# Kernel optimization log

Measured on AMD Instinct MI355X. Metric: run time of the kernel, lower is better.

The kernel has to match this reference:

```python
import jax, jax.numpy as jnp
import numpy as np

N = 100000   # nodes
E = 1600000  # edges (avg degree 16)
D = 128      # in_dim == out_dim (residual path)
NEG_SLOPE = 0.1


def setup_inputs() -> dict:
    key = jax.random.key(0)
    k1, k2, k3 = jax.random.split(key, 3)
    x = jax.random.normal(k1, (N, D), dtype=jnp.float32)
    edge_index = jax.random.randint(k2, (2, E), 0, N, dtype=jnp.int32)
    # GCNConv linear weight (stored as [in, out]; PyG uses x @ W^T with [out, in] — same math)
    W = jax.random.normal(k3, (D, D), dtype=jnp.float32) / np.sqrt(D).astype(np.float32)
    b = jnp.zeros((D,), dtype=jnp.float32)
    return {"x": x, "edge_index": edge_index, "W": W, "b": b}


def reference(x, edge_index, W, b):
    n = x.shape[0]
    # add self loops (GCNConv add_self_loops=True)
    loops = jnp.arange(n, dtype=edge_index.dtype)
    src = jnp.concatenate([edge_index[0], loops])
    dst = jnp.concatenate([edge_index[1], loops])
    # symmetric normalization: deg computed on destination index (PyG gcn_norm)
    deg = jax.ops.segment_sum(jnp.ones_like(dst, dtype=x.dtype), dst, num_segments=n)
    dinv = jnp.where(deg > 0, jax.lax.rsqrt(deg), 0.0)
    norm = dinv[src] * dinv[dst]                     # [E+N]
    # transform-then-propagate: small GEMM, then gather/scale/scatter
    h = x @ W                                        # [N, D]
    msgs = h[src] * norm[:, None]                    # [E+N, D] gather + scale
    agg = jax.ops.segment_sum(msgs, dst, num_segments=n) + b  # scatter-add
    act = jnp.where(agg >= 0, agg, NEG_SLOPE * agg)  # leaky_relu(0.1)
    return act + x                                   # residual (in_dim == out_dim)
```

## Files before the change

kernel.cpp:

```cpp
#include <hip/hip_runtime.h>
#include <hip/hip_bf16.h>

#define D 128
#define NEG_SLOPE 0.1f
#define BSHIFT 7
#define BSIZE 128
#define SRCBITS 17
#define SRCMASK 0x1FFFF
#define NBMAX 784
#define REGION 2432

typedef __attribute__((ext_vector_type(8))) short bf16x8;
typedef __attribute__((ext_vector_type(4))) float f32x4;
typedef __attribute__((ext_vector_type(2))) float f32x2;

__device__ inline unsigned short f2bf(float f) {
    unsigned u = __builtin_bit_cast(unsigned, f);
    u += 0x7fff + ((u >> 16) & 1);
    return (unsigned short)(u >> 16);
}

__global__ __launch_bounds__(512) void k_scatter2(const int* __restrict__ src, const int* __restrict__ dst,
                                                  int* __restrict__ cursor, int* __restrict__ ebuf,
                                                  int E, int NB,
                                                  const float* __restrict__ W,
                                                  unsigned short* __restrict__ Wt) {
    int b = blockIdx.x;
    int nbE = gridDim.x - 32;
    if (b >= nbE) {
        int tt = (b - nbE) * 512 + threadIdx.x;
        int k = tt >> 7, nn = tt & 127;
        Wt[nn * D + k] = f2bf(W[k * D + nn]);
        return;
    }
    __shared__ int cntL[NBMAX], baseL[NBMAX], curL[NBMAX];
    int t = threadIdx.x;
    for (int i = t; i < NB; i += 512) { cntL[i] = 0; curL[i] = 0; }
    __syncthreads();

    const int4* src4 = (const int4*)src;
    const int4* dst4 = (const int4*)dst;
    int sv[8], dv[8];
#pragma unroll
    for (int j = 0; j < 2; j++) {
        int i4 = b * 1024 + j * 512 + t;
        int e = i4 * 4;
        int4 s, d;
        if (e + 4 <= E) {
            s = src4[i4];
            d = dst4[i4];
        } else {
            s.x = (e < E) ? src[e] : 0;     d.x = (e < E) ? dst[e] : -1;
            s.y = (e + 1 < E) ? src[e + 1] : 0; d.y = (e + 1 < E) ? dst[e + 1] : -1;
            s.z = (e + 2 < E) ? src[e + 2] : 0; d.z = (e + 2 < E) ? dst[e + 2] : -1;
            s.w = (e + 3 < E) ? src[e + 3] : 0; d.w = (e + 3 < E) ? dst[e + 3] : -1;
        }
        sv[j * 4 + 0] = s.x; sv[j * 4 + 1] = s.y; sv[j * 4 + 2] = s.z; sv[j * 4 + 3] = s.w;
        dv[j * 4 + 0] = d.x; dv[j * 4 + 1] = d.y; dv[j * 4 + 2] = d.z; dv[j * 4 + 3] = d.w;
    }
#pragma unroll
    for (int k = 0; k < 8; k++)
        if (dv[k] >= 0) atomicAdd(&cntL[dv[k] >> BSHIFT], 1);
    __syncthreads();
    for (int i = t; i < NB; i += 512) {
        int c = cntL[i];
        if (c) baseL[i] = atomicAdd(&cursor[i], c);
    }
    __syncthreads();
#pragma unroll
    for (int k = 0; k < 8; k++) {
        int d = dv[k];
        if (d >= 0) {
            int bk = d >> BSHIFT;
            int slot = baseL[bk] + atomicAdd(&curL[bk], 1);
            if (slot < REGION)
                ebuf[bk * REGION + slot] = ((d & (BSIZE - 1)) << SRCBITS) | sv[k];
        }
    }
}

__global__ __launch_bounds__(256) void k_gemm(const float* __restrict__ x,
                                              const unsigned short* __restrict__ Wt,
                                              const int* __restrict__ bucketCnt,
                                              const int* __restrict__ ebuf,
                                              unsigned char* __restrict__ h, int n) {
    __shared__ unsigned short Wl[D * 136];
    __shared__ int cntL[BSIZE];
    int t = threadIdx.x;
    if (t < BSIZE) cntL[t] = 0;
    const uint4* Wg4 = (const uint4*)Wt;
#pragma unroll
    for (int j = 0; j < 8; j++) {
        int c = t + 256 * j;
        int row = c >> 4, kg = c & 15;
        *(uint4*)&Wl[row * 136 + kg * 8] = Wg4[row * 16 + kg];
    }
    __syncthreads();

    int estart = blockIdx.x * REGION;
    int ecnt = bucketCnt[blockIdx.x];
    if (ecnt > REGION) ecnt = REGION;
    for (int e = t; e < ecnt; e += 256) atomicAdd(&cntL[ebuf[estart + e] >> SRCBITS], 1);

    int lane = t & 63, wave = t >> 6;
    int quad = lane >> 4, mrow = lane & 15;
    int rbase = blockIdx.x * 128 + wave * 32;

    const float4* x4 = (const float4*)x;
    float4 a0[2][4], a1[2][4];
#pragma unroll
    for (int rt = 0; rt < 2; rt++) {
        int row = rbase + rt * 16 + mrow;
        long rowl = (row < n) ? row : (n - 1);
#pragma unroll
        for (int ks = 0; ks < 4; ks++) {
            long base = rowl * 32 + ks * 8 + quad * 2;
            a0[rt][ks] = x4[base];
            a1[rt][ks] = x4[base + 1];
        }
    }
    bf16x8 af[2][4];
#pragma unroll
    for (int rt = 0; rt < 2; rt++)
#pragma unroll
        for (int ks = 0; ks < 4; ks++) {
            bf16x8 f;
            f[0] = (short)f2bf(a0[rt][ks].x); f[1] = (short)f2bf(a0[rt][ks].y);
            f[2] = (short)f2bf(a0[rt][ks].z); f[3] = (short)f2bf(a0[rt][ks].w);
            f[4] = (short)f2bf(a1[rt][ks].x); f[5] = (short)f2bf(a1[rt][ks].y);
            f[6] = (short)f2bf(a1[rt][ks].z); f[7] = (short)f2bf(a1[rt][ks].w);
            af[rt][ks] = f;
        }

    f32x4 acc[2][8];
#pragma unroll
    for (int rt = 0; rt < 2; rt++)
#pragma unroll
        for (int ct = 0; ct < 8; ct++) acc[rt][ct] = (f32x4){0.f, 0.f, 0.f, 0.f};

#pragma unroll
    for (int ks = 0; ks < 4; ks++) {
#pragma unroll
        for (int ct = 0; ct < 8; ct++) {
            bf16x8 bf = *(bf16x8*)&Wl[(ct * 16 + mrow) * 136 + ks * 32 + quad * 8];
#pragma unroll
            for (int rt = 0; rt < 2; rt++)
                acc[rt][ct] = __builtin_amdgcn_mfma_f32_16x16x32_bf16(af[rt][ks], bf, acc[rt][ct], 0, 0, 0);
        }
    }

    __syncthreads();

#pragma unroll
    for (int rt = 0; rt < 2; rt++) {
#pragma unroll
        for (int reg = 0; reg < 4; reg++) {
            int row = rbase + rt * 16 + quad * 4 + reg;
            if (row < n) {
                int rloc = wave * 32 + rt * 16 + quad * 4 + reg;
                float dv = rsqrtf((float)cntL[rloc] + 1.0f);
                float a[8];
#pragma unroll
                for (int ct = 0; ct < 8; ct++) a[ct] = acc[rt][ct][reg] * dv;
                int w0 = __builtin_amdgcn_cvt_pk_fp8_f32(a[0], a[1], 0, false);
                w0 = __builtin_amdgcn_cvt_pk_fp8_f32(a[2], a[3], w0, true);
                int w1 = __builtin_amdgcn_cvt_pk_fp8_f32(a[4], a[5], 0, false);
                w1 = __builtin_amdgcn_cvt_pk_fp8_f32(a[6], a[7], w1, true);
                uint2 wv; wv.x = (unsigned)w0; wv.y = (unsigned)w1;
                *(uint2*)&h[(long)row * 128 + mrow * 8] = wv;
            }
        }
    }
}

#define ACCV(v)                                                       \
    {                                                                 \
        acc2[0] += __builtin_amdgcn_cvt_pk_f32_fp8((int)(v).x, false);\
        acc2[1] += __builtin_amdgcn_cvt_pk_f32_fp8((int)(v).x, true); \
        acc2[2] += __builtin_amdgcn_cvt_pk_f32_fp8((int)(v).y, false);\
        acc2[3] += __builtin_amdgcn_cvt_pk_f32_fp8((int)(v).y, true); \
        acc2[4] += __builtin_amdgcn_cvt_pk_f32_fp8((int)(v).z, false);\
        acc2[5] += __builtin_amdgcn_cvt_pk_f32_fp8((int)(v).z, true); \
        acc2[6] += __builtin_amdgcn_cvt_pk_f32_fp8((int)(v).w, false);\
        acc2[7] += __builtin_amdgcn_cvt_pk_f32_fp8((int)(v).w, true); \
    }

__global__ __launch_bounds__(512) void k_aggregate(const uint4* __restrict__ h4, const float* __restrict__ x,
                                                   const float* __restrict__ bias,
                                                   const int* __restrict__ bucketCnt, const int* __restrict__ ebuf,
                                                   float* __restrict__ out, int N) {
    __shared__ int srcL[REGION];
    __shared__ int degL[BSIZE];
    __shared__ int startL[BSIZE];
    __shared__ int curL[BSIZE];

    int b = blockIdx.x;
    int t = threadIdx.x;
    int nstart = b << BSHIFT;
    int estart = b * REGION;
    int ecnt = bucketCnt[b];
    if (ecnt > REGION) ecnt = REGION;

    if (t < BSIZE) degL[t] = 0;
    __syncthreads();

    int ev[5];
#pragma unroll
    for (int k = 0; k < 5; k++) {
        int e = t + k * 512;
        ev[k] = (e < ecnt) ? ebuf[estart + e] : -1;
    }
#pragma unroll
    for (int k = 0; k < 5; k++)
        if (ev[k] >= 0) atomicAdd(&degL[ev[k] >> SRCBITS], 1);
    __syncthreads();

    if (t < 64) {
        int d0 = degL[2 * t], d1 = degL[2 * t + 1];
        int sum = d0 + d1;
        int inc = sum;
        for (int sh = 1; sh < 64; sh <<= 1) {
            int y = __shfl_up(inc, sh, 64);
            if (t >= sh) inc += y;
        }
        int e0 = inc - sum;
        startL[2 * t] = e0;
        startL[2 * t + 1] = e0 + d0;
        curL[2 * t] = e0;
        curL[2 * t + 1] = e0 + d0;
    }
    __syncthreads();
#pragma unroll
    for (int k = 0; k < 5; k++)
        if (ev[k] >= 0) {
            int v = ev[k];
            int pos = atomicAdd(&curL[v >> SRCBITS], 1);
            srcL[pos] = v & SRCMASK;
        }
    __syncthreads();

    int wave = t >> 6, lane = t & 63;
    int slot = lane >> 3, chunk = lane & 7;
    for (int nloc = wave; nloc < BSIZE; nloc += 8) {
        int i = nstart + nloc;
        if (i >= N) break;
        int start = startL[nloc], m = degL[nloc];

        f32x2 acc2[8];
#pragma unroll
        for (int r = 0; r < 8; r++) acc2[r] = (f32x2){0.f, 0.f};
        if (slot == 0) {
            uint4 v = h4[(long)i * 8 + chunk];
            ACCV(v);
        }

        int j0 = 0;
        if (m >= 16) {
            int ja = start + slot;
            int e0 = srcL[ja], e1 = srcL[ja + 8];
            for (;;) {
                uint4 v0 = h4[(long)e0 * 8 + chunk];
                uint4 v1 = h4[(long)e1 * 8 + chunk];
                j0 += 16;
                bool more = (j0 + 16 <= m);
                if (more) {
                    int jb = start + j0 + slot;
                    e0 = srcL[jb];
                    e1 = srcL[jb + 8];
                }
                ACCV(v0);
                ACCV(v1);
                if (!more) break;
            }
        }
        if (j0 + 8 <= m) {
            int e = srcL[start + j0 + slot];
            uint4 v = h4[(long)e * 8 + chunk];
            ACCV(v);
            j0 += 8;
        }
        for (int j = j0 + slot; j < m; j += 8) {
            int e = srcL[start + j];
            uint4 v = h4[(long)e * 8 + chunk];
            ACCV(v);
        }

#pragma unroll
        for (int r = 0; r < 8; r++) {
            acc2[r].x += __shfl_xor(acc2[r].x, 8, 64);
            acc2[r].x += __shfl_xor(acc2[r].x, 16, 64);
            acc2[r].x += __shfl_xor(acc2[r].x, 32, 64);
            acc2[r].y += __shfl_xor(acc2[r].y, 8, 64);
            acc2[r].y += __shfl_xor(acc2[r].y, 16, 64);
            acc2[r].y += __shfl_xor(acc2[r].y, 32, 64);
        }

        int s1 = slot >> 1;
        f32x2 eL = (s1 == 0) ? acc2[0] : (s1 == 1) ? acc2[1] : (s1 == 2) ? acc2[2] : acc2[3];
        f32x2 eH = (s1 == 0) ? acc2[4] : (s1 == 1) ? acc2[5] : (s1 == 2) ? acc2[6] : acc2[7];
        float ax = (slot & 1) ? eL.y : eL.x;
        float ay = (slot & 1) ? eH.y : eH.x;

        float di = rsqrtf((float)m + 1.0f);
        int dbase = slot * 16 + chunk * 2;
        float2 bb = *(const float2*)&bias[dbase];
        float2 xv = *(const float2*)&x[(long)i * D + dbase];
        ax = ax * di + bb.x;
        ay = ay * di + bb.y;
        ax = (ax >= 0.f) ? ax : NEG_SLOPE * ax;
        ay = (ay >= 0.f) ? ay : NEG_SLOPE * ay;
        float2 o;
        o.x = ax + xv.x;
        o.y = ay + xv.y;
        *(float2*)&out[(long)i * D + dbase] = o;
    }
}

extern "C" void kernel_launch(void* const* d_in, const int* in_sizes, int n_in,
                              void* d_out, int out_size, void* d_ws, size_t ws_size,
                              hipStream_t stream) {
    const float* x = (const float*)d_in[0];
    const int* edge_index = (const int*)d_in[1];
    const float* W = (const float*)d_in[2];
    const float* bias = (const float*)d_in[3];
    float* out = (float*)d_out;

    int N = in_sizes[0] / D;
    int E = in_sizes[1] / 2;
    const int* src = edge_index;
    const int* dst = edge_index + E;
    int NB = (N + BSIZE - 1) >> BSHIFT;

    char* ws = (char*)d_ws;
    size_t off = 0;
    auto alloc = [&](size_t bytes) {
        void* p = ws + off;
        off += (bytes + 15) & ~(size_t)15;
        return p;
    };
    int* cursor = (int*)alloc((size_t)NB * 4);
    int* ebuf = (int*)alloc((size_t)NB * REGION * 4);
    unsigned short* Wt = (unsigned short*)alloc((size_t)D * D * 2);
    unsigned char* h = (unsigned char*)alloc((size_t)N * D);

    int nbE = (E + 4095) / 4096;

    hipMemsetAsync(cursor, 0, (size_t)NB * 4, stream);
    k_scatter2<<<nbE + 32, 512, 0, stream>>>(src, dst, cursor, ebuf, E, NB, W, Wt);
    k_gemm<<<NB, 256, 0, stream>>>(x, Wt, cursor, ebuf, h, N);
    k_aggregate<<<NB, 512, 0, stream>>>((const uint4*)h, x, bias, cursor, ebuf, out, N);
}
```

Baseline: 217.7 us.

## Replace global atomic bucket cursors with per-block sorted runs and CSR build in GEMM

The edge scatter kernel now sorts each 8192-edge chunk locally in shared memory by destination bucket and writes contiguous runs plus per-bucket offsets, so the global cursor atomics and the memset go away. The GEMM kernel gathers its bucket's runs from every chunk, computes degrees, builds a per-node CSR (start, degree, sorted sources) and writes it out. The aggregate kernel becomes one wave per node that reads the prebuilt CSR. The intent is to remove global atomics and scattered writes and to spread aggregation across many small blocks. The cost is that each GEMM block scans about 196 run descriptors twice with serial per-thread loops, plus extra global CSR traffic.

```diff
diff --git a/kernel.cpp b/kernel.cpp
--- a/kernel.cpp
+++ b/kernel.cpp
@@ -8,7 +8,9 @@
 #define SRCBITS 17
 #define SRCMASK 0x1FFFF
 #define NBMAX 784
-#define REGION 2432
+#define NBPAD 1024
+#define EPB 8192
+#define REGION2 2432
 
 typedef __attribute__((ext_vector_type(8))) short bf16x8;
 typedef __attribute__((ext_vector_type(4))) float f32x4;
@@ -21,7 +23,7 @@
 }
 
 __global__ __launch_bounds__(512) void k_scatter2(const int* __restrict__ src, const int* __restrict__ dst,
-                                                  int* __restrict__ cursor, int* __restrict__ ebuf,
+                                                  int* __restrict__ runs, int* __restrict__ ebuf,
                                                   int E, int NB,
                                                   const float* __restrict__ W,
                                                   unsigned short* __restrict__ Wt) {
@@ -33,24 +35,29 @@
         Wt[nn * D + k] = f2bf(W[k * D + nn]);
         return;
     }
-    __shared__ int cntL[NBMAX], baseL[NBMAX], curL[NBMAX];
+    __shared__ int cntL[NBPAD];
+    __shared__ int baseL[NBPAD];
+    __shared__ int curL[NBMAX];
+    __shared__ int stageV[EPB];
+    __shared__ int wsum[8];
+
     int t = threadIdx.x;
-    for (int i = t; i < NB; i += 512) { cntL[i] = 0; curL[i] = 0; }
+    for (int i = t; i < NBPAD; i += 512) cntL[i] = 0;
     __syncthreads();
 
     const int4* src4 = (const int4*)src;
     const int4* dst4 = (const int4*)dst;
-    int sv[8], dv[8];
-#pragma unroll
-    for (int j = 0; j < 2; j++) {
-        int i4 = b * 1024 + j * 512 + t;
+    int sv[16], dv[16];
+#pragma unroll
+    for (int j = 0; j < 4; j++) {
+        int i4 = b * 2048 + j * 512 + t;
         int e = i4 * 4;
         int4 s, d;
         if (e + 4 <= E) {
             s = src4[i4];
             d = dst4[i4];
         } else {
-            s.x = (e < E) ? src[e] : 0;     d.x = (e < E) ? dst[e] : -1;
+            s.x = (e < E) ? src[e] : 0;         d.x = (e < E) ? dst[e] : -1;
             s.y = (e + 1 < E) ? src[e + 1] : 0; d.y = (e + 1 < E) ? dst[e + 1] : -1;
             s.z = (e + 2 < E) ? src[e + 2] : 0; d.z = (e + 2 < E) ? dst[e + 2] : -1;
             s.w = (e + 3 < E) ? src[e + 3] : 0; d.w = (e + 3 < E) ? dst[e + 3] : -1;
@@ -59,34 +66,71 @@
         dv[j * 4 + 0] = d.x; dv[j * 4 + 1] = d.y; dv[j * 4 + 2] = d.z; dv[j * 4 + 3] = d.w;
     }
 #pragma unroll
-    for (int k = 0; k < 8; k++)
+    for (int k = 0; k < 16; k++)
         if (dv[k] >= 0) atomicAdd(&cntL[dv[k] >> BSHIFT], 1);
     __syncthreads();
-    for (int i = t; i < NB; i += 512) {
-        int c = cntL[i];
-        if (c) baseL[i] = atomicAdd(&cursor[i], c);
-    }
-    __syncthreads();
-#pragma unroll
-    for (int k = 0; k < 8; k++) {
+
+    {
+        int lane = t & 63, wave = t >> 6;
+        int c0 = cntL[2 * t], c1 = cntL[2 * t + 1];
+        int sum = c0 + c1;
+        int inc = sum;
+        for (int sh = 1; sh < 64; sh <<= 1) {
+            int y = __shfl_up(inc, sh, 64);
+            if (lane >= sh) inc += y;
+        }
+        int texcl = inc - sum;
+        if (lane == 63) wsum[wave] = inc;
+        __syncthreads();
+        int woff = 0;
+        for (int w = 0; w < wave; w++) woff += wsum[w];
+        int e0 = woff + texcl;
+        baseL[2 * t] = e0;
+        baseL[2 * t + 1] = e0 + c0;
+        if (2 * t < NB) curL[2 * t] = e0;
+        if (2 * t + 1 < NB) curL[2 * t + 1] = e0 + c0;
+    }
+    __syncthreads();
+
+    long rrow = (long)b * (NB + 1);
+    for (int bb = t; bb < NB; bb += 512) runs[rrow + bb] = baseL[bb];
+    if (t == 0) {
+        int cnt = E - b * EPB;
+        if (cnt > EPB) cnt = EPB;
+        runs[rrow + NB] = cnt;
+    }
+
+#pragma unroll
+    for (int k = 0; k < 16; k++) {
         int d = dv[k];
         if (d >= 0) {
-            int bk = d >> BSHIFT;
-            int slot = baseL[bk] + atomicAdd(&curL[bk], 1);
-            if (slot < REGION)
-                ebuf[bk * REGION + slot] = ((d & (BSIZE - 1)) << SRCBITS) | sv[k];
-        }
-    }
+            int pos = atomicAdd(&curL[d >> BSHIFT], 1);
+            stageV[pos] = ((d & (BSIZE - 1)) << SRCBITS) | sv[k];
+        }
+    }
+    __syncthreads();
+
+    int4* eb4 = (int4*)&ebuf[(long)b * EPB];
+    const int4* st4 = (const int4*)stageV;
+#pragma unroll
+    for (int j = 0; j < 4; j++) eb4[j * 512 + t] = st4[j * 512 + t];
 }
 
 __global__ __launch_bounds__(256) void k_gemm(const float* __restrict__ x,
                                               const unsigned short* __restrict__ Wt,
-                                              const int* __restrict__ bucketCnt,
-                                              const int* __restrict__ ebuf,
-                                              unsigned char* __restrict__ h, int n) {
+                                              const int* __restrict__ runs, const int* __restrict__ ebuf,
+                                              int nbE,
+                                              int* __restrict__ startA, int* __restrict__ degA,
+                                              int* __restrict__ sorted_src,
+                                              unsigned char* __restrict__ h, int n, int NB) {
     __shared__ unsigned short Wl[D * 136];
     __shared__ int cntL[BSIZE];
+    __shared__ int startL[BSIZE];
+    __shared__ int curL[BSIZE];
+    __shared__ int srcL[REGION2];
+
     int t = threadIdx.x;
+    int b = blockIdx.x;
     if (t < BSIZE) cntL[t] = 0;
     const uint4* Wg4 = (const uint4*)Wt;
 #pragma unroll
@@ -97,14 +141,9 @@
     }
     __syncthreads();
 
-    int estart = blockIdx.x * REGION;
-    int ecnt = bucketCnt[blockIdx.x];
-    if (ecnt > REGION) ecnt = REGION;
-    for (int e = t; e < ecnt; e += 256) atomicAdd(&cntL[ebuf[estart + e] >> SRCBITS], 1);
-
     int lane = t & 63, wave = t >> 6;
     int quad = lane >> 4, mrow = lane & 15;
-    int rbase = blockIdx.x * 128 + wave * 32;
+    int rbase = b * 128 + wave * 32;
 
     const float4* x4 = (const float4*)x;
     float4 a0[2][4], a1[2][4];
@@ -119,6 +158,16 @@
             a1[rt][ks] = x4[base + 1];
         }
     }
+
+    int NBP = NB + 1;
+    for (int i = t; i < nbE; i += 256) {
+        long rrow = (long)i * NBP;
+        int rs = runs[rrow + b], re = runs[rrow + b + 1];
+        const int* ep = ebuf + (long)i * EPB;
+        for (int e = rs; e < re; e++) atomicAdd(&cntL[ep[e] >> SRCBITS], 1);
+    }
+    __syncthreads();
+
     bf16x8 af[2][4];
 #pragma unroll
     for (int rt = 0; rt < 2; rt++)
@@ -132,6 +181,46 @@
             af[rt][ks] = f;
         }
 
+    if (t < 64) {
+        int d0 = cntL[2 * t], d1 = cntL[2 * t + 1];
+        int sum = d0 + d1;
+        int inc = sum;
+        for (int sh = 1; sh < 64; sh <<= 1) {
+            int y = __shfl_up(inc, sh, 64);
+            if (t >= sh) inc += y;
+        }
+        int e0 = inc - sum;
+        startL[2 * t] = e0;
+        startL[2 * t + 1] = e0 + d0;
+        curL[2 * t] = e0;
+        curL[2 * t + 1] = e0 + d0;
+    }
+    __syncthreads();
+
+    if (t < BSIZE) {
+        int i = b * BSIZE + t;
+        if (i < n) {
+            startA[i] = b * REGION2 + startL[t];
+            degA[i] = cntL[t];
+        }
+    }
+
+    for (int i = t; i < nbE; i += 256) {
+        long rrow = (long)i * NBP;
+        int rs = runs[rrow + b], re = runs[rrow + b + 1];
+        const int* ep = ebuf + (long)i * EPB;
+        for (int e = rs; e < re; e++) {
+            int v = ep[e];
+            int pos = atomicAdd(&curL[v >> SRCBITS], 1);
+            if (pos < REGION2) srcL[pos] = v & SRCMASK;
+        }
+    }
+    __syncthreads();
+
+    int ecnt = startL[BSIZE - 1] + cntL[BSIZE - 1];
+    if (ecnt > REGION2) ecnt = REGION2;
+    for (int e = t; e < ecnt; e += 256) sorted_src[(long)b * REGION2 + e] = srcL[e];
+
     f32x4 acc[2][8];
 #pragma unroll
     for (int rt = 0; rt < 2; rt++)
@@ -148,8 +237,6 @@
                 acc[rt][ct] = __builtin_amdgcn_mfma_f32_16x16x32_bf16(af[rt][ks], bf, acc[rt][ct], 0, 0, 0);
         }
     }
-
-    __syncthreads();
 
 #pragma unroll
     for (int rt = 0; rt < 2; rt++) {
@@ -185,135 +272,84 @@
         acc2[7] += __builtin_amdgcn_cvt_pk_f32_fp8((int)(v).w, true); \
     }
 
-__global__ __launch_bounds__(512) void k_aggregate(const uint4* __restrict__ h4, const float* __restrict__ x,
+__global__ __launch_bounds__(256) void k_aggregate(const uint4* __restrict__ h4, const float* __restrict__ x,
                                                    const float* __restrict__ bias,
-                                                   const int* __restrict__ bucketCnt, const int* __restrict__ ebuf,
-                                                   float* __restrict__ out, int N) {
-    __shared__ int srcL[REGION];
-    __shared__ int degL[BSIZE];
-    __shared__ int startL[BSIZE];
-    __shared__ int curL[BSIZE];
-
-    int b = blockIdx.x;
-    int t = threadIdx.x;
-    int nstart = b << BSHIFT;
-    int estart = b * REGION;
-    int ecnt = bucketCnt[b];
-    if (ecnt > REGION) ecnt = REGION;
-
-    if (t < BSIZE) degL[t] = 0;
-    __syncthreads();
-
-    int ev[5];
-#pragma unroll
-    for (int k = 0; k < 5; k++) {
-        int e = t + k * 512;
-        ev[k] = (e < ecnt) ? ebuf[estart + e] : -1;
-    }
-#pragma unroll
-    for (int k = 0; k < 5; k++)
-        if (ev[k] >= 0) atomicAdd(&degL[ev[k] >> SRCBITS], 1);
-    __syncthreads();
-
-    if (t < 64) {
-        int d0 = degL[2 * t], d1 = degL[2 * t + 1];
-        int sum = d0 + d1;
-        int inc = sum;
-        for (int sh = 1; sh < 64; sh <<= 1) {
-            int y = __shfl_up(inc, sh, 64);
-            if (t >= sh) inc += y;
-        }
-        int e0 = inc - sum;
-        startL[2 * t] = e0;
-        startL[2 * t + 1] = e0 + d0;
-        curL[2 * t] = e0;
-        curL[2 * t + 1] = e0 + d0;
-    }
-    __syncthreads();
-#pragma unroll
-    for (int k = 0; k < 5; k++)
-        if (ev[k] >= 0) {
-            int v = ev[k];
-            int pos = atomicAdd(&curL[v >> SRCBITS], 1);
-            srcL[pos] = v & SRCMASK;
-        }
-    __syncthreads();
-
-    int wave = t >> 6, lane = t & 63;
+                                                   const int* __restrict__ startA, const int* __restrict__ degA,
+                                                   const int* __restrict__ sorted_src,
+                                                   float* __restrict__ out, int n) {
+    int wave = threadIdx.x >> 6, lane = threadIdx.x & 63;
+    int i = blockIdx.x * 4 + wave;
+    if (i >= n) return;
     int slot = lane >> 3, chunk = lane & 7;
-    for (int nloc = wave; nloc < BSIZE; nloc += 8) {
-        int i = nstart + nloc;
-        if (i >= N) break;
-        int start = startL[nloc], m = degL[nloc];
-
-        f32x2 acc2[8];
-#pragma unroll
-        for (int r = 0; r < 8; r++) acc2[r] = (f32x2){0.f, 0.f};
-        if (slot == 0) {
-            uint4 v = h4[(long)i * 8 + chunk];
-            ACCV(v);
-        }
-
-        int j0 = 0;
-        if (m >= 16) {
-            int ja = start + slot;
-            int e0 = srcL[ja], e1 = srcL[ja + 8];
-            for (;;) {
-                uint4 v0 = h4[(long)e0 * 8 + chunk];
-                uint4 v1 = h4[(long)e1 * 8 + chunk];
-                j0 += 16;
-                bool more = (j0 + 16 <= m);
-                if (more) {
-                    int jb = start + j0 + slot;
-                    e0 = srcL[jb];
-                    e1 = srcL[jb + 8];
-                }
-                ACCV(v0);
-                ACCV(v1);
-                if (!more) break;
+    int start = startA[i], m = degA[i];
+
+    f32x2 acc2[8];
+#pragma unroll
+    for (int r = 0; r < 8; r++) acc2[r] = (f32x2){0.f, 0.f};
+    if (slot == 0) {
+        uint4 v = h4[(long)i * 8 + chunk];
+        ACCV(v);
+    }
+
+    int j0 = 0;
+    if (m >= 16) {
+        int ja = start + slot;
+        int e0 = sorted_src[ja], e1 = sorted_src[ja + 8];
+        for (;;) {
+            uint4 v0 = h4[(long)e0 * 8 + chunk];
+            uint4 v1 = h4[(long)e1 * 8 + chunk];
+            j0 += 16;
+            bool more = (j0 + 16 <= m);
+            if (more) {
+                int jb = start + j0 + slot;
+                e0 = sorted_src[jb];
+                e1 = sorted_src[jb + 8];
             }
-        }
-        if (j0 + 8 <= m) {
-            int e = srcL[start + j0 + slot];
-            uint4 v = h4[(long)e * 8 + chunk];
-            ACCV(v);
-            j0 += 8;
-        }
-        for (int j = j0 + slot; j < m; j += 8) {
-            int e = srcL[start + j];
-            uint4 v = h4[(long)e * 8 + chunk];
-            ACCV(v);
-        }
-
-#pragma unroll
-        for (int r = 0; r < 8; r++) {
-            acc2[r].x += __shfl_xor(acc2[r].x, 8, 64);
-            acc2[r].x += __shfl_xor(acc2[r].x, 16, 64);
-            acc2[r].x += __shfl_xor(acc2[r].x, 32, 64);
-            acc2[r].y += __shfl_xor(acc2[r].y, 8, 64);
-            acc2[r].y += __shfl_xor(acc2[r].y, 16, 64);
-            acc2[r].y += __shfl_xor(acc2[r].y, 32, 64);
-        }
-
-        int s1 = slot >> 1;
-        f32x2 eL = (s1 == 0) ? acc2[0] : (s1 == 1) ? acc2[1] : (s1 == 2) ? acc2[2] : acc2[3];
-        f32x2 eH = (s1 == 0) ? acc2[4] : (s1 == 1) ? acc2[5] : (s1 == 2) ? acc2[6] : acc2[7];
-        float ax = (slot & 1) ? eL.y : eL.x;
-        float ay = (slot & 1) ? eH.y : eH.x;
-
-        float di = rsqrtf((float)m + 1.0f);
-        int dbase = slot * 16 + chunk * 2;
-        float2 bb = *(const float2*)&bias[dbase];
-        float2 xv = *(const float2*)&x[(long)i * D + dbase];
-        ax = ax * di + bb.x;
-        ay = ay * di + bb.y;
-        ax = (ax >= 0.f) ? ax : NEG_SLOPE * ax;
-        ay = (ay >= 0.f) ? ay : NEG_SLOPE * ay;
-        float2 o;
-        o.x = ax + xv.x;
-        o.y = ay + xv.y;
-        *(float2*)&out[(long)i * D + dbase] = o;
-    }
+            ACCV(v0);
+            ACCV(v1);
+            if (!more) break;
+        }
+    }
+    if (j0 + 8 <= m) {
+        int e = sorted_src[start + j0 + slot];
+        uint4 v = h4[(long)e * 8 + chunk];
+        ACCV(v);
+        j0 += 8;
+    }
+    for (int j = j0 + slot; j < m; j += 8) {
+        int e = sorted_src[start + j];
+        uint4 v = h4[(long)e * 8 + chunk];
+        ACCV(v);
+    }
+
+#pragma unroll
+    for (int r = 0; r < 8; r++) {
+        acc2[r].x += __shfl_xor(acc2[r].x, 8, 64);
+        acc2[r].x += __shfl_xor(acc2[r].x, 16, 64);
+        acc2[r].x += __shfl_xor(acc2[r].x, 32, 64);
+        acc2[r].y += __shfl_xor(acc2[r].y, 8, 64);
+        acc2[r].y += __shfl_xor(acc2[r].y, 16, 64);
+        acc2[r].y += __shfl_xor(acc2[r].y, 32, 64);
+    }
+
+    int s1 = slot >> 1;
+    f32x2 eL = (s1 == 0) ? acc2[0] : (s1 == 1) ? acc2[1] : (s1 == 2) ? acc2[2] : acc2[3];
+    f32x2 eH = (s1 == 0) ? acc2[4] : (s1 == 1) ? acc2[5] : (s1 == 2) ? acc2[6] : acc2[7];
+    float ax = (slot & 1) ? eL.y : eL.x;
+    float ay = (slot & 1) ? eH.y : eH.x;
+
+    float di = rsqrtf((float)m + 1.0f);
+    int dbase = slot * 16 + chunk * 2;
+    float2 bb = *(const float2*)&bias[dbase];
+    float2 xv = *(const float2*)&x[(long)i * D + dbase];
+    ax = ax * di + bb.x;
+    ay = ay * di + bb.y;
+    ax = (ax >= 0.f) ? ax : NEG_SLOPE * ax;
+    ay = (ay >= 0.f) ? ay : NEG_SLOPE * ay;
+    float2 o;
+    o.x = ax + xv.x;
+    o.y = ay + xv.y;
+    *(float2*)&out[(long)i * D + dbase] = o;
 }
 
 extern "C" void kernel_launch(void* const* d_in, const int* in_sizes, int n_in,
@@ -330,6 +366,7 @@
     const int* src = edge_index;
     const int* dst = edge_index + E;
     int NB = (N + BSIZE - 1) >> BSHIFT;
+    int nbE = (E + EPB - 1) / EPB;
 
     char* ws = (char*)d_ws;
     size_t off = 0;
@@ -338,15 +375,15 @@
         off += (bytes + 15) & ~(size_t)15;
         return p;
     };
-    int* cursor = (int*)alloc((size_t)NB * 4);
-    int* ebuf = (int*)alloc((size_t)NB * REGION * 4);
+    int* runs = (int*)alloc((size_t)nbE * (NB + 1) * 4);
+    int* ebuf = (int*)alloc((size_t)nbE * EPB * 4);
+    int* startA = (int*)alloc((size_t)N * 4);
+    int* degA = (int*)alloc((size_t)N * 4);
+    int* sorted_src = (int*)alloc((size_t)NB * REGION2 * 4);
     unsigned short* Wt = (unsigned short*)alloc((size_t)D * D * 2);
     unsigned char* h = (unsigned char*)alloc((size_t)N * D);
 
-    int nbE = (E + 4095) / 4096;
-
-    hipMemsetAsync(cursor, 0, (size_t)NB * 4, stream);
-    k_scatter2<<<nbE + 32, 512, 0, stream>>>(src, dst, cursor, ebuf, E, NB, W, Wt);
-    k_gemm<<<NB, 256, 0, stream>>>(x, Wt, cursor, ebuf, h, N);
-    k_aggregate<<<NB, 512, 0, stream>>>((const uint4*)h, x, bias, cursor, ebuf, out, N);
-}
+    k_scatter2<<<nbE + 32, 512, 0, stream>>>(src, dst, runs, ebuf, E, NB, W, Wt);
+    k_gemm<<<NB, 256, 0, stream>>>(x, Wt, runs, ebuf, nbE, startA, degA, sorted_src, h, N, NB);
+    k_aggregate<<<(N + 3) / 4, 256, 0, stream>>>((const uint4*)h, x, bias, startA, degA, sorted_src, out, N);
+}
```

Measured after the change: 205.3 us. -5.7%, faster.

## Overlap GEMM with edge bucketing and move source normalization into aggregation

Applied to the files above, without the earlier changes.

Merges the edge-bucketing scatter and the x@W GEMM into one launch whose blocks split between the two tasks, so GEMM no longer waits on the scatter. The GEMM writes unscaled fp8 h, and a new CSR kernel sorts edges per bucket to global memory and emits per-node start, degree and dinv. Aggregation then runs one wave per node and applies dinv[src] per edge through an extra gather. This removes the separate W transpose and the degree count inside the GEMM, at the cost of an extra kernel, extra global traffic for sorted_src, and an additional random dinv load per edge. fp8 h is now unscaled, which changes quantization error.

```diff
diff --git a/kernel.cpp b/kernel.cpp
--- a/kernel.cpp
+++ b/kernel.cpp
@@ -9,6 +9,7 @@
 #define SRCMASK 0x1FFFF
 #define NBMAX 784
 #define REGION 2432
+#define EPBS 4096
 
 typedef __attribute__((ext_vector_type(8))) short bf16x8;
 typedef __attribute__((ext_vector_type(4))) float f32x4;
@@ -20,37 +21,116 @@
     return (unsigned short)(u >> 16);
 }
 
-__global__ __launch_bounds__(512) void k_scatter2(const int* __restrict__ src, const int* __restrict__ dst,
-                                                  int* __restrict__ cursor, int* __restrict__ ebuf,
-                                                  int E, int NB,
-                                                  const float* __restrict__ W,
-                                                  unsigned short* __restrict__ Wt) {
+__global__ __launch_bounds__(256) void k_pre(const float* __restrict__ x, const float* __restrict__ W,
+                                             const int* __restrict__ src, const int* __restrict__ dst,
+                                             int* __restrict__ cursor, int* __restrict__ ebuf,
+                                             unsigned char* __restrict__ h,
+                                             int E, int NB, int n) {
+    __shared__ __align__(16) unsigned char lds_u[34816];
     int b = blockIdx.x;
-    int nbE = gridDim.x - 32;
-    if (b >= nbE) {
-        int tt = (b - nbE) * 512 + threadIdx.x;
-        int k = tt >> 7, nn = tt & 127;
-        Wt[nn * D + k] = f2bf(W[k * D + nn]);
+    int t = threadIdx.x;
+
+    if (b < NB) {
+        unsigned short* Wl = (unsigned short*)lds_u;
+        const float4* W4 = (const float4*)W;
+#pragma unroll
+        for (int j = 0; j < 16; j++) {
+            int e4 = j * 256 + t;
+            float4 w = W4[e4];
+            int e = e4 * 4;
+            int k = e >> 7, n0 = e & 127;
+            Wl[(n0 + 0) * 136 + k] = f2bf(w.x);
+            Wl[(n0 + 1) * 136 + k] = f2bf(w.y);
+            Wl[(n0 + 2) * 136 + k] = f2bf(w.z);
+            Wl[(n0 + 3) * 136 + k] = f2bf(w.w);
+        }
+        __syncthreads();
+
+        int lane = t & 63, wave = t >> 6;
+        int quad = lane >> 4, mrow = lane & 15;
+        int rbase = b * 128 + wave * 32;
+
+        const float4* x4 = (const float4*)x;
+        float4 a0[2][4], a1[2][4];
+#pragma unroll
+        for (int rt = 0; rt < 2; rt++) {
+            int row = rbase + rt * 16 + mrow;
+            long rowl = (row < n) ? row : (n - 1);
+#pragma unroll
+            for (int ks = 0; ks < 4; ks++) {
+                long base = rowl * 32 + ks * 8 + quad * 2;
+                a0[rt][ks] = x4[base];
+                a1[rt][ks] = x4[base + 1];
+            }
+        }
+        bf16x8 af[2][4];
+#pragma unroll
+        for (int rt = 0; rt < 2; rt++)
+#pragma unroll
+            for (int ks = 0; ks < 4; ks++) {
+                bf16x8 f;
+                f[0] = (short)f2bf(a0[rt][ks].x); f[1] = (short)f2bf(a0[rt][ks].y);
+                f[2] = (short)f2bf(a0[rt][ks].z); f[3] = (short)f2bf(a0[rt][ks].w);
+                f[4] = (short)f2bf(a1[rt][ks].x); f[5] = (short)f2bf(a1[rt][ks].y);
+                f[6] = (short)f2bf(a1[rt][ks].z); f[7] = (short)f2bf(a1[rt][ks].w);
+                af[rt][ks] = f;
+            }
+
+        f32x4 acc[2][8];
+#pragma unroll
+        for (int rt = 0; rt < 2; rt++)
+#pragma unroll
+            for (int ct = 0; ct < 8; ct++) acc[rt][ct] = (f32x4){0.f, 0.f, 0.f, 0.f};
+
+#pragma unroll
+        for (int ks = 0; ks < 4; ks++) {
+#pragma unroll
+            for (int ct = 0; ct < 8; ct++) {
+                bf16x8 bf = *(bf16x8*)&Wl[(ct * 16 + mrow) * 136 + ks * 32 + quad * 8];
+#pragma unroll
+                for (int rt = 0; rt < 2; rt++)
+                    acc[rt][ct] = __builtin_amdgcn_mfma_f32_16x16x32_bf16(af[rt][ks], bf, acc[rt][ct], 0, 0, 0);
+            }
+        }
+
+#pragma unroll
+        for (int rt = 0; rt < 2; rt++) {
+#pragma unroll
+            for (int reg = 0; reg < 4; reg++) {
+                int row = rbase + rt * 16 + quad * 4 + reg;
+                if (row < n) {
+                    int w0 = __builtin_amdgcn_cvt_pk_fp8_f32(acc[rt][0][reg], acc[rt][1][reg], 0, false);
+                    w0 = __builtin_amdgcn_cvt_pk_fp8_f32(acc[rt][2][reg], acc[rt][3][reg], w0, true);
+                    int w1 = __builtin_amdgcn_cvt_pk_fp8_f32(acc[rt][4][reg], acc[rt][5][reg], 0, false);
+                    w1 = __builtin_amdgcn_cvt_pk_fp8_f32(acc[rt][6][reg], acc[rt][7][reg], w1, true);
+                    uint2 wv; wv.x = (unsigned)w0; wv.y = (unsigned)w1;
+                    *(uint2*)&h[(long)row * 128 + mrow * 8] = wv;
+                }
+            }
+        }
         return;
     }
-    __shared__ int cntL[NBMAX], baseL[NBMAX], curL[NBMAX];
-    int t = threadIdx.x;
-    for (int i = t; i < NB; i += 512) { cntL[i] = 0; curL[i] = 0; }
+
+    int sb = b - NB;
+    int* cntL = (int*)lds_u;
+    int* baseL = cntL + NBMAX;
+    int* curL = baseL + NBMAX;
+    for (int i = t; i < NB; i += 256) { cntL[i] = 0; }
     __syncthreads();
 
     const int4* src4 = (const int4*)src;
     const int4* dst4 = (const int4*)dst;
-    int sv[8], dv[8];
-#pragma unroll
-    for (int j = 0; j < 2; j++) {
-        int i4 = b * 1024 + j * 512 + t;
+    int sv[16], dv[16];
+#pragma unroll
+    for (int j = 0; j < 4; j++) {
+        int i4 = sb * 1024 + j * 256 + t;
         int e = i4 * 4;
         int4 s, d;
         if (e + 4 <= E) {
             s = src4[i4];
             d = dst4[i4];
         } else {
-            s.x = (e < E) ? src[e] : 0;     d.x = (e < E) ? dst[e] : -1;
+            s.x = (e < E) ? src[e] : 0;         d.x = (e < E) ? dst[e] : -1;
             s.y = (e + 1 < E) ? src[e + 1] : 0; d.y = (e + 1 < E) ? dst[e + 1] : -1;
             s.z = (e + 2 < E) ? src[e + 2] : 0; d.z = (e + 2 < E) ? dst[e + 2] : -1;
             s.w = (e + 3 < E) ? src[e + 3] : 0; d.w = (e + 3 < E) ? dst[e + 3] : -1;
@@ -59,164 +139,55 @@
         dv[j * 4 + 0] = d.x; dv[j * 4 + 1] = d.y; dv[j * 4 + 2] = d.z; dv[j * 4 + 3] = d.w;
     }
 #pragma unroll
-    for (int k = 0; k < 8; k++)
+    for (int k = 0; k < 16; k++)
         if (dv[k] >= 0) atomicAdd(&cntL[dv[k] >> BSHIFT], 1);
     __syncthreads();
-    for (int i = t; i < NB; i += 512) {
+    for (int i = t; i < NB; i += 256) {
         int c = cntL[i];
         if (c) baseL[i] = atomicAdd(&cursor[i], c);
-    }
-    __syncthreads();
-#pragma unroll
-    for (int k = 0; k < 8; k++) {
+        curL[i] = 0;
+    }
+    __syncthreads();
+#pragma unroll
+    for (int k = 0; k < 16; k++) {
         int d = dv[k];
         if (d >= 0) {
             int bk = d >> BSHIFT;
             int slot = baseL[bk] + atomicAdd(&curL[bk], 1);
             if (slot < REGION)
-                ebuf[bk * REGION + slot] = ((d & (BSIZE - 1)) << SRCBITS) | sv[k];
-        }
-    }
-}
-
-__global__ __launch_bounds__(256) void k_gemm(const float* __restrict__ x,
-                                              const unsigned short* __restrict__ Wt,
-                                              const int* __restrict__ bucketCnt,
-                                              const int* __restrict__ ebuf,
-                                              unsigned char* __restrict__ h, int n) {
-    __shared__ unsigned short Wl[D * 136];
-    __shared__ int cntL[BSIZE];
-    int t = threadIdx.x;
+                ebuf[(long)bk * REGION + slot] = ((d & (BSIZE - 1)) << SRCBITS) | sv[k];
+        }
+    }
+}
+
+__global__ __launch_bounds__(256) void k_csr(const int* __restrict__ cursor, const int* __restrict__ ebuf,
+                                             int* __restrict__ startA, int* __restrict__ degA,
+                                             float* __restrict__ dinvA, int* __restrict__ sorted_src,
+                                             int N) {
+    __shared__ int srcL[REGION];
+    __shared__ int cntL[BSIZE], startL[BSIZE], curL[BSIZE];
+
+    int b = blockIdx.x, t = threadIdx.x;
+    long estart = (long)b * REGION;
+    int ecnt = cursor[b];
+    if (ecnt > REGION) ecnt = REGION;
+
     if (t < BSIZE) cntL[t] = 0;
-    const uint4* Wg4 = (const uint4*)Wt;
-#pragma unroll
-    for (int j = 0; j < 8; j++) {
-        int c = t + 256 * j;
-        int row = c >> 4, kg = c & 15;
-        *(uint4*)&Wl[row * 136 + kg * 8] = Wg4[row * 16 + kg];
-    }
-    __syncthreads();
-
-    int estart = blockIdx.x * REGION;
-    int ecnt = bucketCnt[blockIdx.x];
-    if (ecnt > REGION) ecnt = REGION;
-    for (int e = t; e < ecnt; e += 256) atomicAdd(&cntL[ebuf[estart + e] >> SRCBITS], 1);
-
-    int lane = t & 63, wave = t >> 6;
-    int quad = lane >> 4, mrow = lane & 15;
-    int rbase = blockIdx.x * 128 + wave * 32;
-
-    const float4* x4 = (const float4*)x;
-    float4 a0[2][4], a1[2][4];
-#pragma unroll
-    for (int rt = 0; rt < 2; rt++) {
-        int row = rbase + rt * 16 + mrow;
-        long rowl = (row < n) ? row : (n - 1);
-#pragma unroll
-        for (int ks = 0; ks < 4; ks++) {
-            long base = rowl * 32 + ks * 8 + quad * 2;
-            a0[rt][ks] = x4[base];
-            a1[rt][ks] = x4[base + 1];
-        }
-    }
-    bf16x8 af[2][4];
-#pragma unroll
-    for (int rt = 0; rt < 2; rt++)
-#pragma unroll
-        for (int ks = 0; ks < 4; ks++) {
-            bf16x8 f;
-            f[0] = (short)f2bf(a0[rt][ks].x); f[1] = (short)f2bf(a0[rt][ks].y);
-            f[2] = (short)f2bf(a0[rt][ks].z); f[3] = (short)f2bf(a0[rt][ks].w);
-            f[4] = (short)f2bf(a1[rt][ks].x); f[5] = (short)f2bf(a1[rt][ks].y);
-            f[6] = (short)f2bf(a1[rt][ks].z); f[7] = (short)f2bf(a1[rt][ks].w);
-            af[rt][ks] = f;
-        }
-
-    f32x4 acc[2][8];
-#pragma unroll
-    for (int rt = 0; rt < 2; rt++)
-#pragma unroll
-        for (int ct = 0; ct < 8; ct++) acc[rt][ct] = (f32x4){0.f, 0.f, 0.f, 0.f};
-
-#pragma unroll
-    for (int ks = 0; ks < 4; ks++) {
-#pragma unroll
-        for (int ct = 0; ct < 8; ct++) {
-            bf16x8 bf = *(bf16x8*)&Wl[(ct * 16 + mrow) * 136 + ks * 32 + quad * 8];
-#pragma unroll
-            for (int rt = 0; rt < 2; rt++)
-                acc[rt][ct] = __builtin_amdgcn_mfma_f32_16x16x32_bf16(af[rt][ks], bf, acc[rt][ct], 0, 0, 0);
-        }
-    }
-
-    __syncthreads();
-
-#pragma unroll
-    for (int rt = 0; rt < 2; rt++) {
-#pragma unroll
-        for (int reg = 0; reg < 4; reg++) {
-            int row = rbase + rt * 16 + quad * 4 + reg;
-            if (row < n) {
-                int rloc = wave * 32 + rt * 16 + quad * 4 + reg;
-                float dv = rsqrtf((float)cntL[rloc] + 1.0f);
-                float a[8];
-#pragma unroll
-                for (int ct = 0; ct < 8; ct++) a[ct] = acc[rt][ct][reg] * dv;
-                int w0 = __builtin_amdgcn_cvt_pk_fp8_f32(a[0], a[1], 0, false);
-                w0 = __builtin_amdgcn_cvt_pk_fp8_f32(a[2], a[3], w0, true);
-                int w1 = __builtin_amdgcn_cvt_pk_fp8_f32(a[4], a[5], 0, false);
-                w1 = __builtin_amdgcn_cvt_pk_fp8_f32(a[6], a[7], w1, true);
-                uint2 wv; wv.x = (unsigned)w0; wv.y = (unsigned)w1;
-                *(uint2*)&h[(long)row * 128 + mrow * 8] = wv;
-            }
-        }
-    }
-}
-
-#define ACCV(v)                                                       \
-    {                                                                 \
-        acc2[0] += __builtin_amdgcn_cvt_pk_f32_fp8((int)(v).x, false);\
-        acc2[1] += __builtin_amdgcn_cvt_pk_f32_fp8((int)(v).x, true); \
-        acc2[2] += __builtin_amdgcn_cvt_pk_f32_fp8((int)(v).y, false);\
-        acc2[3] += __builtin_amdgcn_cvt_pk_f32_fp8((int)(v).y, true); \
-        acc2[4] += __builtin_amdgcn_cvt_pk_f32_fp8((int)(v).z, false);\
-        acc2[5] += __builtin_amdgcn_cvt_pk_f32_fp8((int)(v).z, true); \
-        acc2[6] += __builtin_amdgcn_cvt_pk_f32_fp8((int)(v).w, false);\
-        acc2[7] += __builtin_amdgcn_cvt_pk_f32_fp8((int)(v).w, true); \
-    }
-
-__global__ __launch_bounds__(512) void k_aggregate(const uint4* __restrict__ h4, const float* __restrict__ x,
-                                                   const float* __restrict__ bias,
-                                                   const int* __restrict__ bucketCnt, const int* __restrict__ ebuf,
-                                                   float* __restrict__ out, int N) {
-    __shared__ int srcL[REGION];
-    __shared__ int degL[BSIZE];
-    __shared__ int startL[BSIZE];
-    __shared__ int curL[BSIZE];
-
-    int b = blockIdx.x;
-    int t = threadIdx.x;
-    int nstart = b << BSHIFT;
-    int estart = b * REGION;
-    int ecnt = bucketCnt[b];
-    if (ecnt > REGION) ecnt = REGION;
-
-    if (t < BSIZE) degL[t] = 0;
-    __syncthreads();
-
-    int ev[5];
-#pragma unroll
-    for (int k = 0; k < 5; k++) {
-        int e = t + k * 512;
+    __syncthreads();
+
+    int ev[10];
+#pragma unroll
+    for (int k = 0; k < 10; k++) {
+        int e = t + k * 256;
         ev[k] = (e < ecnt) ? ebuf[estart + e] : -1;
     }
 #pragma unroll
-    for (int k = 0; k < 5; k++)
-        if (ev[k] >= 0) atomicAdd(&degL[ev[k] >> SRCBITS], 1);
+    for (int k = 0; k < 10; k++)
+        if (ev[k] >= 0) atomicAdd(&cntL[ev[k] >> SRCBITS], 1);
     __syncthreads();
 
     if (t < 64) {
-        int d0 = degL[2 * t], d1 = degL[2 * t + 1];
+        int d0 = cntL[2 * t], d1 = cntL[2 * t + 1];
         int sum = d0 + d1;
         int inc = sum;
         for (int sh = 1; sh < 64; sh <<= 1) {
@@ -230,8 +201,18 @@
         curL[2 * t + 1] = e0 + d0;
     }
     __syncthreads();
-#pragma unroll
-    for (int k = 0; k < 5; k++)
+
+    if (t < BSIZE) {
+        int i = b * BSIZE + t;
+        if (i < N) {
+            startA[i] = b * REGION + startL[t];
+            degA[i] = cntL[t];
+            dinvA[i] = rsqrtf((float)cntL[t] + 1.0f);
+        }
+    }
+
+#pragma unroll
+    for (int k = 0; k < 10; k++)
         if (ev[k] >= 0) {
             int v = ev[k];
             int pos = atomicAdd(&curL[v >> SRCBITS], 1);
@@ -239,81 +220,105 @@
         }
     __syncthreads();
 
-    int wave = t >> 6, lane = t & 63;
+    for (int e = t; e < ecnt; e += 256) sorted_src[estart + e] = srcL[e];
+}
+
+#define ACCVS(v, s)                                                           \
+    {                                                                         \
+        acc2[0] += __builtin_amdgcn_cvt_pk_f32_fp8((int)(v).x, false) * (s);  \
+        acc2[1] += __builtin_amdgcn_cvt_pk_f32_fp8((int)(v).x, true) * (s);   \
+        acc2[2] += __builtin_amdgcn_cvt_pk_f32_fp8((int)(v).y, false) * (s);  \
+        acc2[3] += __builtin_amdgcn_cvt_pk_f32_fp8((int)(v).y, true) * (s);   \
+        acc2[4] += __builtin_amdgcn_cvt_pk_f32_fp8((int)(v).z, false) * (s);  \
+        acc2[5] += __builtin_amdgcn_cvt_pk_f32_fp8((int)(v).z, true) * (s);   \
+        acc2[6] += __builtin_amdgcn_cvt_pk_f32_fp8((int)(v).w, false) * (s);  \
+        acc2[7] += __builtin_amdgcn_cvt_pk_f32_fp8((int)(v).w, true) * (s);   \
+    }
+
+__global__ __launch_bounds__(256) void k_aggregate(const uint4* __restrict__ h4, const float* __restrict__ x,
+                                                   const float* __restrict__ bias,
+                                                   const int* __restrict__ startA, const int* __restrict__ degA,
+                                                   const float* __restrict__ dinvA,
+                                                   const int* __restrict__ sorted_src,
+                                                   float* __restrict__ out, int n) {
+    int wave = threadIdx.x >> 6, lane = threadIdx.x & 63;
+    int i = blockIdx.x * 4 + wave;
+    if (i >= n) return;
     int slot = lane >> 3, chunk = lane & 7;
-    for (int nloc = wave; nloc < BSIZE; nloc += 8) {
-        int i = nstart + nloc;
-        if (i >= N) break;
-        int start = startL[nloc], m = degL[nloc];
-
-        f32x2 acc2[8];
-#pragma unroll
-        for (int r = 0; r < 8; r++) acc2[r] = (f32x2){0.f, 0.f};
-        if (slot == 0) {
-            uint4 v = h4[(long)i * 8 + chunk];
-            ACCV(v);
-        }
-
-        int j0 = 0;
-        if (m >= 16) {
-            int ja = start + slot;
-            int e0 = srcL[ja], e1 = srcL[ja + 8];
-            for (;;) {
-                uint4 v0 = h4[(long)e0 * 8 + chunk];
-                uint4 v1 = h4[(long)e1 * 8 + chunk];
-                j0 += 16;
-                bool more = (j0 + 16 <= m);
-                if (more) {
-                    int jb = start + j0 + slot;
-                    e0 = srcL[jb];
-                    e1 = srcL[jb + 8];
-                }
-                ACCV(v0);
-                ACCV(v1);
-                if (!more) break;
-            }
-        }
-        if (j0 + 8 <= m) {
-            int e = srcL[start + j0 + slot];
-            uint4 v = h4[(long)e * 8 + chunk];
-            ACCV(v);
-            j0 += 8;
-        }
-        for (int j = j0 + slot; j < m; j += 8) {
-            int e = srcL[start + j];
-            uint4 v = h4[(long)e * 8 + chunk];
-            ACCV(v);
-        }
-
-#pragma unroll
-        for (int r = 0; r < 8; r++) {
-            acc2[r].x += __shfl_xor(acc2[r].x, 8, 64);
-            acc2[r].x += __shfl_xor(acc2[r].x, 16, 64);
-            acc2[r].x += __shfl_xor(acc2[r].x, 32, 64);
-            acc2[r].y += __shfl_xor(acc2[r].y, 8, 64);
-            acc2[r].y += __shfl_xor(acc2[r].y, 16, 64);
-            acc2[r].y += __shfl_xor(acc2[r].y, 32, 64);
-        }
-
-        int s1 = slot >> 1;
-        f32x2 eL = (s1 == 0) ? acc2[0] : (s1 == 1) ? acc2[1] : (s1 == 2) ? acc2[2] : acc2[3];
-        f32x2 eH = (s1 == 0) ? acc2[4] : (s1 == 1) ? acc2[5] : (s1 == 2) ? acc2[6] : acc2[7];
-        float ax = (slot & 1) ? eL.y : eL.x;
-        float ay = (slot & 1) ? eH.y : eH.x;
-
-        float di = rsqrtf((float)m + 1.0f);
-        int dbase = slot * 16 + chunk * 2;
-        float2 bb = *(const float2*)&bias[dbase];
-        float2 xv = *(const float2*)&x[(long)i * D + dbase];
-        ax = ax * di + bb.x;
-        ay = ay * di + bb.y;
-        ax = (ax >= 0.f) ? ax : NEG_SLOPE * ax;
-        ay = (ay >= 0.f) ? ay : NEG_SLOPE * ay;
-        float2 o;
-        o.x = ax + xv.x;
-        o.y = ay + xv.y;
-        *(float2*)&out[(long)i * D + dbase] = o;
-    }
+    int start = startA[i], m = degA[i];
+    float di = rsqrtf((float)m + 1.0f);
+
+    f32x2 acc2[8];
+#pragma unroll
+    for (int r = 0; r < 8; r++) acc2[r] = (f32x2){0.f, 0.f};
+    if (slot == 0) {
+        uint4 v = h4[(long)i * 8 + chunk];
+        ACCVS(v, di);
+    }
+
+    int j0 = 0;
+    if (m >= 16) {
+        int ja = start + slot;
+        int e0 = sorted_src[ja], e1 = sorted_src[ja + 8];
+        float dv0 = dinvA[e0], dv1 = dinvA[e1];
+        for (;;) {
+            uint4 v0 = h4[(long)e0 * 8 + chunk];
+            uint4 v1 = h4[(long)e1 * 8 + chunk];
+            j0 += 16;
+            bool more = (j0 + 16 <= m);
+            if (more) {
+                int jb = start + j0 + slot;
+                e0 = sorted_src[jb];
+                e1 = sorted_src[jb + 8];
+            }
+            ACCVS(v0, dv0);
+            ACCVS(v1, dv1);
+            if (!more) break;
+            dv0 = dinvA[e0];
+            dv1 = dinvA[e1];
+        }
+    }
+    if (j0 + 8 <= m) {
+        int e = sorted_src[start + j0 + slot];
+        float dv = dinvA[e];
+        uint4 v = h4[(long)e * 8 + chunk];
+        ACCVS(v, dv);
+        j0 += 8;
+    }
+    for (int j = j0 + slot; j < m; j += 8) {
+        int e = sorted_src[start + j];
+        float dv = dinvA[e];
+        uint4 v = h4[(long)e * 8 + chunk];
+        ACCVS(v, dv);
+    }
+
+#pragma unroll
+    for (int r = 0; r < 8; r++) {
+        acc2[r].x += __shfl_xor(acc2[r].x, 8, 64);
+        acc2[r].x += __shfl_xor(acc2[r].x, 16, 64);
+        acc2[r].x += __shfl_xor(acc2[r].x, 32, 64);
+        acc2[r].y += __shfl_xor(acc2[r].y, 8, 64);
+        acc2[r].y += __shfl_xor(acc2[r].y, 16, 64);
+        acc2[r].y += __shfl_xor(acc2[r].y, 32, 64);
+    }
+
+    int s1 = slot >> 1;
+    f32x2 eL = (s1 == 0) ? acc2[0] : (s1 == 1) ? acc2[1] : (s1 == 2) ? acc2[2] : acc2[3];
+    f32x2 eH = (s1 == 0) ? acc2[4] : (s1 == 1) ? acc2[5] : (s1 == 2) ? acc2[6] : acc2[7];
+    float ax = (slot & 1) ? eL.y : eL.x;
+    float ay = (slot & 1) ? eH.y : eH.x;
+
+    int dbase = slot * 16 + chunk * 2;
+    float2 bb = *(const float2*)&bias[dbase];
+    float2 xv = *(const float2*)&x[(long)i * D + dbase];
+    ax = ax * di + bb.x;
+    ay = ay * di + bb.y;
+    ax = (ax >= 0.f) ? ax : NEG_SLOPE * ax;
+    ay = (ay >= 0.f) ? ay : NEG_SLOPE * ay;
+    float2 o;
+    o.x = ax + xv.x;
+    o.y = ay + xv.y;
+    *(float2*)&out[(long)i * D + dbase] = o;
 }
 
 extern "C" void kernel_launch(void* const* d_in, const int* in_sizes, int n_in,
@@ -330,6 +335,7 @@
     const int* src = edge_index;
     const int* dst = edge_index + E;
     int NB = (N + BSIZE - 1) >> BSHIFT;
+    int nbE = (E + EPBS - 1) / EPBS;
 
     char* ws = (char*)d_ws;
     size_t off = 0;
@@ -340,13 +346,14 @@
     };
     int* cursor = (int*)alloc((size_t)NB * 4);
     int* ebuf = (int*)alloc((size_t)NB * REGION * 4);
-    unsigned short* Wt = (unsigned short*)alloc((size_t)D * D * 2);
+    int* startA = (int*)alloc((size_t)N * 4);
+    int* degA = (int*)alloc((size_t)N * 4);
+    float* dinvA = (float*)alloc((size_t)N * 4);
+    int* sorted_src = (int*)alloc((size_t)NB * REGION * 4);
     unsigned char* h = (unsigned char*)alloc((size_t)N * D);
 
-    int nbE = (E + 4095) / 4096;
-
     hipMemsetAsync(cursor, 0, (size_t)NB * 4, stream);
-    k_scatter2<<<nbE + 32, 512, 0, stream>>>(src, dst, cursor, ebuf, E, NB, W, Wt);
-    k_gemm<<<NB, 256, 0, stream>>>(x, Wt, cursor, ebuf, h, N);
-    k_aggregate<<<NB, 512, 0, stream>>>((const uint4*)h, x, bias, cursor, ebuf, out, N);
-}
+    k_pre<<<NB + nbE, 256, 0, stream>>>(x, W, src, dst, cursor, ebuf, h, E, NB, N);
+    k_csr<<<NB, 256, 0, stream>>>(cursor, ebuf, startA, degA, dinvA, sorted_src, N);
+    k_aggregate<<<(N + 3) / 4, 256, 0, stream>>>((const uint4*)h, x, bias, startA, degA, dinvA, sorted_src, out, N);
+}
```

Result: faster. 199.3 us (-8.4%).
